# Optimization experiments

Hardware: AMD Instinct MI355X
Metric: run time of the kernel (lower is better)

The kernel has to match this reference:

```python
import jax, jax.numpy as jnp
import numpy as np

NEG_SLOPE = 0.2  # PyG GATConv default leaky_relu slope


def _gat_layer(x, W, att_src, att_dst, bias, src, dst, num_nodes, heads, out_c, concat):
    # x: [N, F_in] -> h: [N, H, C]
    h = (x @ W).reshape(num_nodes, heads, out_c)
    a_src = jnp.einsum('nhc,hc->nh', h, att_src)  # [N, H]
    a_dst = jnp.einsum('nhc,hc->nh', h, att_dst)  # [N, H]
    # edge (src -> dst): attention logit per edge/head
    e = jax.nn.leaky_relu(a_src[src] + a_dst[dst], NEG_SLOPE)  # [E, H]
    # softmax over edges sharing the same destination node
    m = jax.ops.segment_max(e, dst, num_segments=num_nodes)  # [N, H]
    m = jnp.where(jnp.isfinite(m), m, 0.0)
    ex = jnp.exp(e - m[dst])
    denom = jax.ops.segment_sum(ex, dst, num_segments=num_nodes)  # [N, H]
    alpha = ex / (denom[dst] + 1e-16)  # [E, H]
    # weighted scatter-add aggregation
    msg = h[src] * alpha[:, :, None]  # [E, H, C]
    out = jax.ops.segment_sum(msg, dst, num_segments=num_nodes)  # [N, H, C]
    if concat:
        out = out.reshape(num_nodes, heads * out_c)
    else:
        out = out.mean(axis=1)
    return out + bias


def _add_self_loops(edge_index, num_nodes):
    loop = jnp.arange(num_nodes, dtype=edge_index.dtype)
    src = jnp.concatenate([edge_index[0], loop])
    dst = jnp.concatenate([edge_index[1], loop])
    return src, dst


def setup_inputs() -> dict:
    key = jax.random.key(0)
    ks = jax.random.split(key, 9)
    N, F_in, E, H, C, OUT = 30000, 256, 300000, 8, 128, 64
    x = jax.random.normal(ks[0], (N, F_in), dtype=jnp.float32)
    edge_index = jax.random.randint(ks[1], (2, E), 0, N, dtype=jnp.int32)
    s1 = 1.0 / np.sqrt(F_in)
    s2 = 1.0 / np.sqrt(H * C)
    return {
        'x': x,
        'edge_index': edge_index,
        'W1': jax.random.normal(ks[2], (F_in, H * C), dtype=jnp.float32) * s1,
        'att_src1': jax.random.normal(ks[3], (H, C), dtype=jnp.float32) * s2,
        'att_dst1': jax.random.normal(ks[4], (H, C), dtype=jnp.float32) * s2,
        'b1': jnp.zeros((H * C,), dtype=jnp.float32),
        'W2': jax.random.normal(ks[5], (H * C, OUT), dtype=jnp.float32) * s2,
        'att_src2': jax.random.normal(ks[6], (1, OUT), dtype=jnp.float32) * 0.125,
        'att_dst2': jax.random.normal(ks[7], (1, OUT), dtype=jnp.float32) * 0.125,
        'b2': jnp.zeros((OUT,), dtype=jnp.float32),
    }


def reference(x, edge_index, W1, att_src1, att_dst1, b1, W2, att_src2, att_dst2, b2):
    N = x.shape[0]
    src, dst = _add_self_loops(edge_index, N)
    # dropout layers are identity in eval mode
    h = _gat_layer(x, W1, att_src1, att_dst1, b1, src, dst, N, 8, 128, True)
    h = jax.nn.elu(h)
    out = _gat_layer(h, W2, att_src2, att_dst2, b2, src, dst, N, 1, 64, False)
    return jax.nn.log_softmax(out, axis=-1)
```

## Files before the change

### kernel.cpp

```cpp
#include <hip/hip_runtime.h>
#include <math.h>

#define N_NODES 30000
#define F_IN 256
#define E_RAW 300000
#define E_TOT (E_RAW + N_NODES)
#define HEADS 8
#define CH 128
#define HC 1024
#define OUTC 64
#define NEG_SLOPE 0.2f
#define CAP 64

typedef __attribute__((ext_vector_type(8))) short bf16x8;
typedef __attribute__((ext_vector_type(4))) float f32x4;
typedef __attribute__((ext_vector_type(2))) float f32x2;

__device__ __forceinline__ float bf2f(unsigned short u) {
    return __uint_as_float(((unsigned)u) << 16);
}
__device__ __forceinline__ unsigned short f2bf(float f) {
    unsigned b = __float_as_uint(f);
    b += 0x7FFFu + ((b >> 16) & 1u);
    return (unsigned short)(b >> 16);
}
__device__ __forceinline__ void edge_sd(const int* __restrict__ ei, int e, int& s, int& d) {
    if (e < E_RAW) { s = ei[e]; d = ei[E_RAW + e]; }
    else           { s = e - E_RAW; d = s; }
}
__device__ __forceinline__ void async_cp16(const void* g, void* l) {
    __builtin_amdgcn_global_load_lds((const __attribute__((address_space(1))) void*)g,
                                     (__attribute__((address_space(3))) void*)l, 16, 0, 0);
}
__device__ __forceinline__ int slotP(int s) {
    return ((s >> 6) << 6) + ((s >> 2) & 15) + ((s & 3) << 4);
}
__device__ __forceinline__ void wave_sync() {
    __builtin_amdgcn_fence(__ATOMIC_ACQ_REL, "wavefront");
    __builtin_amdgcn_wave_barrier();
}

#define NB_CVTX (N_NODES * F_IN / 4 / 256)
#define NB_DEG  ((E_TOT + 255) / 256)
#define NB_W1T  ((F_IN * HC + 255) / 256)
#define NB_W2T  ((HC * OUTC + 255) / 256)
#define NB_PREP (NB_CVTX + NB_DEG + NB_W1T + NB_W2T)

__global__ __launch_bounds__(256)
void prep_kernel(const float* __restrict__ x, unsigned short* __restrict__ xb,
                 const float* __restrict__ W1, unsigned short* __restrict__ W1t,
                 const float* __restrict__ W2, unsigned short* __restrict__ W2t,
                 const int* __restrict__ ei, int* __restrict__ deg)
{
    const int b = blockIdx.x, t = threadIdx.x;
    if (b < NB_CVTX) {
        int i = b * 256 + t;
        const float4 v = reinterpret_cast<const float4*>(x)[i];
        ushort4 o;
        o.x = f2bf(v.x); o.y = f2bf(v.y); o.z = f2bf(v.z); o.w = f2bf(v.w);
        reinterpret_cast<ushort4*>(xb)[i] = o;
    } else if (b < NB_CVTX + NB_DEG) {
        int e = (b - NB_CVTX) * 256 + t;
        if (e < E_TOT) {
            int s, d; edge_sd(ei, e, s, d);
            atomicAdd(&deg[d], 1);
        }
    } else if (b < NB_CVTX + NB_DEG + NB_W1T) {
        int i = (b - NB_CVTX - NB_DEG) * 256 + t;
        if (i < F_IN * HC) {
            int k = i >> 10, n = i & (HC - 1);
            W1t[n * F_IN + k] = f2bf(W1[i]);
        }
    } else {
        int i = (b - NB_CVTX - NB_DEG - NB_W1T) * 256 + t;
        if (i < HC * OUTC) {
            int s = i >> 6, n = i & (OUTC - 1);
            W2t[n * HC + s] = f2bf(W2[slotP(s) * OUTC + n]);
        }
    }
}

__global__ __launch_bounds__(256)
void gemm1_mfma(const unsigned short* __restrict__ A,
                const unsigned short* __restrict__ Bt,
                unsigned* __restrict__ Cp,
                const float* __restrict__ att_src, const float* __restrict__ att_dst,
                float* __restrict__ a_src, float* __restrict__ a_dst, int M)
{
    __shared__ unsigned short Al[128 * 64];
    __shared__ unsigned short Bl[128 * 64];
    __shared__ float s_src[128][2];
    __shared__ float s_dst[128][2];
    const int tid  = threadIdx.x;
    const int wave = tid >> 6, lane = tid & 63;
    const int quad = lane >> 4, l16 = lane & 15;
    const int wr = (wave >> 1) * 64, wc = (wave & 1) * 64;
    const int row0 = blockIdx.y * 128;
    const int col0 = blockIdx.x * 128;

    f32x4 acc[4][4];
#pragma unroll
    for (int i = 0; i < 4; i++)
#pragma unroll
        for (int j = 0; j < 4; j++) acc[i][j] = (f32x4){0.f, 0.f, 0.f, 0.f};

    for (int k0 = 0; k0 < F_IN; k0 += 64) {
#pragma unroll
        for (int p = 0; p < 4; p++) {
            int idx = tid + 256 * p;
            int r = idx >> 3, q = idx & 7;
            async_cp16(A + (size_t)(row0 + r) * F_IN + k0 + ((q ^ (r & 7)) * 8),
                       Al + (size_t)(wave * 64 + 256 * p) * 8);
        }
#pragma unroll
        for (int p = 0; p < 4; p++) {
            int idx = tid + 256 * p;
            int r = idx >> 3, q = idx & 7;
            async_cp16(Bt + (size_t)(col0 + r) * F_IN + k0 + ((q ^ (r & 7)) * 8),
                       Bl + (size_t)(wave * 64 + 256 * p) * 8);
        }
        __syncthreads();
#pragma unroll
        for (int kh = 0; kh < 2; kh++) {
            const int cx = (kh * 4 + quad) ^ (l16 & 7);
            bf16x8 af[4], bg[4];
#pragma unroll
            for (int i = 0; i < 4; i++)
                af[i] = *reinterpret_cast<const bf16x8*>(Al + ((wr + i * 16 + l16) * 8 + cx) * 8);
#pragma unroll
            for (int j = 0; j < 4; j++)
                bg[j] = *reinterpret_cast<const bf16x8*>(Bl + ((wc + j * 16 + l16) * 8 + cx) * 8);
#pragma unroll
            for (int i = 0; i < 4; i++)
#pragma unroll
                for (int j = 0; j < 4; j++)
                    acc[i][j] = __builtin_amdgcn_mfma_f32_16x16x32_bf16(af[i], bg[j], acc[i][j], 0, 0, 0);
        }
        __syncthreads();
    }
    const int D = ((col0 + wc) >> 6) * 16 + l16;
#pragma unroll
    for (int i = 0; i < 4; i++) {
#pragma unroll
        for (int r = 0; r < 4; r++) {
            int row = row0 + wr + i * 16 + quad * 4 + r;
            if (row >= M) continue;
            int w8 = __builtin_amdgcn_cvt_pk_fp8_f32(acc[i][0][r], acc[i][1][r], 0, false);
            w8 = __builtin_amdgcn_cvt_pk_fp8_f32(acc[i][2][r], acc[i][3][r], w8, true);
            Cp[(size_t)row * 256 + D] = (unsigned)w8;
        }
    }
    const float* asv = att_src + blockIdx.x * CH;
    const float* adv = att_dst + blockIdx.x * CH;
    float av[4], dv[4];
#pragma unroll
    for (int j = 0; j < 4; j++) {
        av[j] = asv[wc + j * 16 + l16];
        dv[j] = adv[wc + j * 16 + l16];
    }
#pragma unroll
    for (int i = 0; i < 4; i++) {
#pragma unroll
        for (int r = 0; r < 4; r++) {
            float ps = 0.f, pd = 0.f;
#pragma unroll
            for (int j = 0; j < 4; j++) {
                float cc = acc[i][j][r];
                ps += cc * av[j];
                pd += cc * dv[j];
            }
#pragma unroll
            for (int o = 1; o < 16; o <<= 1) {
                ps += __shfl_xor(ps, o);
                pd += __shfl_xor(pd, o);
            }
            if (l16 == 0) {
                int lr = wr + i * 16 + quad * 4 + r;
                s_src[lr][wc >> 6] = ps;
                s_dst[lr][wc >> 6] = pd;
            }
        }
    }
    __syncthreads();
    if (tid < 128) {
        int row = row0 + tid;
        if (row < M) {
            a_src[row * 8 + blockIdx.x] = s_src[tid][0] + s_src[tid][1];
            a_dst[row * 8 + blockIdx.x] = s_dst[tid][0] + s_dst[tid][1];
        }
    }
}

__global__ __launch_bounds__(256)
void gemm2_mfma(const unsigned short* __restrict__ A,
                const unsigned short* __restrict__ Bt,
                unsigned short* __restrict__ C,
                const float* __restrict__ att_src2, const float* __restrict__ att_dst2,
                float* __restrict__ a_src2, float* __restrict__ a_dst2, int M)
{
    __shared__ unsigned short Al[64 * 64];
    __shared__ unsigned short Bl[64 * 64];
    const int tid  = threadIdx.x;
    const int wave = tid >> 6, lane = tid & 63;
    const int quad = lane >> 4, l16 = lane & 15;
    const int wr = wave * 16;
    const int row0 = blockIdx.x * 64;

    f32x4 acc[4];
#pragma unroll
    for (int j = 0; j < 4; j++) acc[j] = (f32x4){0.f, 0.f, 0.f, 0.f};

    for (int k0 = 0; k0 < HC; k0 += 64) {
#pragma unroll
        for (int p = 0; p < 2; p++) {
            int idx = tid + 256 * p;
            int r = idx >> 3, q = idx & 7;
            async_cp16(A + (size_t)(row0 + r) * HC + k0 + ((q ^ (r & 7)) * 8),
                       Al + (size_t)(wave * 64 + 256 * p) * 8);
        }
#pragma unroll
        for (int p = 0; p < 2; p++) {
            int idx = tid + 256 * p;
            int r = idx >> 3, q = idx & 7;
            async_cp16(Bt + (size_t)r * HC + k0 + ((q ^ (r & 7)) * 8),
                       Bl + (size_t)(wave * 64 + 256 * p) * 8);
        }
        __syncthreads();
#pragma unroll
        for (int kh = 0; kh < 2; kh++) {
            const int cx = (kh * 4 + quad) ^ (l16 & 7);
            bf16x8 af, bg[4];
            af = *reinterpret_cast<const bf16x8*>(Al + ((wr + l16) * 8 + cx) * 8);
#pragma unroll
            for (int j = 0; j < 4; j++)
                bg[j] = *reinterpret_cast<const bf16x8*>(Bl + ((j * 16 + l16) * 8 + cx) * 8);
#pragma unroll
            for (int j = 0; j < 4; j++)
                acc[j] = __builtin_amdgcn_mfma_f32_16x16x32_bf16(af, bg[j], acc[j], 0, 0, 0);
        }
        __syncthreads();
    }
    float av[4], dv[4];
#pragma unroll
    for (int j = 0; j < 4; j++) {
        av[j] = att_src2[j * 16 + l16];
        dv[j] = att_dst2[j * 16 + l16];
    }
#pragma unroll
    for (int r = 0; r < 4; r++) {
        int row = row0 + wr + quad * 4 + r;
        float ps = 0.f, pd = 0.f;
#pragma unroll
        for (int j = 0; j < 4; j++) {
            float cc = acc[j][r];
            int col = j * 16 + l16;
            if (row < M) C[(size_t)row * OUTC + col] = f2bf(cc);
            ps += cc * av[j];
            pd += cc * dv[j];
        }
#pragma unroll
        for (int o = 1; o < 16; o <<= 1) {
            ps += __shfl_xor(ps, o);
            pd += __shfl_xor(pd, o);
        }
        if (l16 == 0 && row < M) {
            a_src2[row] = ps;
            a_dst2[row] = pd;
        }
    }
}

__global__ __launch_bounds__(256)
void alloc_kernel(const int* __restrict__ deg, int* __restrict__ rowstart,
                  int* __restrict__ cursor, int* __restrict__ counter)
{
    int d = blockIdx.x * 256 + threadIdx.x;
    int lane = threadIdx.x & 63;
    int v = (d < N_NODES) ? deg[d] : 0;
    int x = v;
#pragma unroll
    for (int o = 1; o < 64; o <<= 1) {
        int y = __shfl_up(x, o);
        if (lane >= o) x += y;
    }
    int excl = x - v;
    int total = __shfl(x, 63);
    int base = 0;
    if (lane == 63) base = atomicAdd(counter, total);
    base = __shfl(base, 63);
    if (d < N_NODES) {
        rowstart[d] = base + excl;
        cursor[d]   = base + excl;
    }
}

__global__ void scatter_kernel(const int* __restrict__ ei, int* __restrict__ cursor,
                               int* __restrict__ csr_src)
{
    int e = blockIdx.x * 256 + threadIdx.x;
    if (e >= E_TOT) return;
    int s, d; edge_sd(ei, e, s, d);
    int pos = atomicAdd(&cursor[d], 1);
    csr_src[pos] = s;
}

__global__ __launch_bounds__(256)
void agg1_fused(const int* __restrict__ rowstart, const int* __restrict__ degv,
                const int* __restrict__ csr_src,
                const unsigned* __restrict__ h1p,
                const float* __restrict__ a_src1, const float* __restrict__ a_dst1,
                const float* __restrict__ b1, unsigned short* __restrict__ out1)
{
    const int t   = threadIdx.x;
    const int sub = t >> 6;
    const int tl  = t & 63;
    const int h   = tl >> 3;
    const int d   = blockIdx.x * 4 + sub;

    __shared__ float exps[4][CAP * 8];
    __shared__ int   srcs[4][CAP];

    const int start = rowstart[d];
    const int deg   = degv[d];

    const float adst = a_dst1[d * 8 + h];
    const uint4* __restrict__ h1v = reinterpret_cast<const uint4*>(h1p);

    float denom_part = 0.f;
    float acc[16];
#pragma unroll
    for (int k = 0; k < 16; k++) acc[k] = 0.f;

    for (int c0 = 0; c0 < deg; c0 += CAP) {
        const int cend = min(deg - c0, CAP);
        for (int c = (tl & 7); c < cend; c += 8) {
            int s = csr_src[start + c0 + c];
            if (h == 0) srcs[sub][c] = s;
            float a = a_src1[s * 8 + h] + adst;
            float v = a > 0.f ? a : NEG_SLOPE * a;
            float ex = __expf(v);
            exps[sub][c * 8 + h] = ex;
            denom_part += ex;
        }
        wave_sync();
        {
            int   s_cur = srcs[sub][0];
            float w_cur = exps[sub][h];
            uint4 u_cur = h1v[(size_t)s_cur * 64 + tl];
            for (int c = 0; c < cend; c++) {
                int   s_nxt = 0; float w_nxt = 0.f; uint4 u_nxt;
                if (c + 1 < cend) {
                    s_nxt = srcs[sub][c + 1];
                    w_nxt = exps[sub][(c + 1) * 8 + h];
                    u_nxt = h1v[(size_t)s_nxt * 64 + tl];
                }
#pragma unroll
                for (int dw = 0; dw < 4; dw++) {
                    unsigned wd = (&u_cur.x)[dw];
                    f32x2 lo = __builtin_amdgcn_cvt_pk_f32_fp8((int)wd, false);
                    f32x2 hi = __builtin_amdgcn_cvt_pk_f32_fp8((int)wd, true);
                    acc[dw * 4 + 0] += w_cur * lo.x;
                    acc[dw * 4 + 1] += w_cur * lo.y;
                    acc[dw * 4 + 2] += w_cur * hi.x;
                    acc[dw * 4 + 3] += w_cur * hi.y;
                }
                s_cur = s_nxt; w_cur = w_nxt; u_cur = u_nxt;
            }
        }
        wave_sync();
    }
#pragma unroll
    for (int o = 1; o < 8; o <<= 1) denom_part += __shfl_xor(denom_part, o);
    const float dinv = 1.f / (denom_part + 1e-16f);

    unsigned short ov[16];
#pragma unroll
    for (int e = 0; e < 16; e++) {
        float v = acc[e] * dinv + b1[slotP(16 * tl + e)];
        v = v > 0.f ? v : __expf(v) - 1.f;
        ov[e] = f2bf(v);
    }
    uint4* op = reinterpret_cast<uint4*>(out1 + (size_t)d * HC + 16 * tl);
    op[0] = *reinterpret_cast<uint4*>(&ov[0]);
    op[1] = *reinterpret_cast<uint4*>(&ov[8]);
}

__global__ __launch_bounds__(256)
void agg2_lsm(const int* __restrict__ rowstart, const int* __restrict__ degv,
              const int* __restrict__ csr_src,
              const unsigned short* __restrict__ h2,
              const float* __restrict__ a_src2, const float* __restrict__ a_dst2,
              const float* __restrict__ b2, float* __restrict__ out)
{
    const int t = threadIdx.x;
    const int sub  = t >> 6;
    const int lane = t & 63;
    const int eo   = lane >> 4;
    const int cq   = lane & 15;
    const int d = blockIdx.x * 4 + sub;

    __shared__ float exs[4][CAP];
    __shared__ int   ss[4][CAP];

    const int start = rowstart[d];
    const int deg   = degv[d];

    const float adst = a_dst2[d];
    const uint2* __restrict__ h2v = reinterpret_cast<const uint2*>(h2);
    float denom_part = 0.f;
    float ax = 0.f, ay = 0.f, az = 0.f, aw = 0.f;

    for (int c0 = 0; c0 < deg; c0 += CAP) {
        const int cend = min(deg - c0, CAP);
        for (int c = lane; c < cend; c += 64) {
            int s = csr_src[start + c0 + c];
            ss[sub][c] = s;
            float a = a_src2[s] + adst;
            float v = a > 0.f ? a : NEG_SLOPE * a;
            float ex = __expf(v);
            exs[sub][c] = ex;
            denom_part += ex;
        }
        wave_sync();
        {
            int   cc = eo;
            float w0 = (cc < cend) ? exs[sub][cc] : 0.f;
            int   s0 = (cc < cend) ? ss[sub][cc] : ss[sub][0];
            uint2 u0 = h2v[(size_t)s0 * 16 + cq];
            for (int c = 0; c + 4 < cend; c += 4) {
                int cc1 = c + 4 + eo;
                float w1 = (cc1 < cend) ? exs[sub][cc1] : 0.f;
                int   s1 = (cc1 < cend) ? ss[sub][cc1] : ss[sub][0];
                uint2 u1 = h2v[(size_t)s1 * 16 + cq];
                ax += w0 * __uint_as_float(u0.x << 16);
                ay += w0 * __uint_as_float(u0.x & 0xFFFF0000u);
                az += w0 * __uint_as_float(u0.y << 16);
                aw += w0 * __uint_as_float(u0.y & 0xFFFF0000u);
                w0 = w1; s0 = s1; u0 = u1;
            }
            ax += w0 * __uint_as_float(u0.x << 16);
            ay += w0 * __uint_as_float(u0.x & 0xFFFF0000u);
            az += w0 * __uint_as_float(u0.y << 16);
            aw += w0 * __uint_as_float(u0.y & 0xFFFF0000u);
        }
        wave_sync();
    }
    ax += __shfl_xor(ax, 16); ax += __shfl_xor(ax, 32);
    ay += __shfl_xor(ay, 16); ay += __shfl_xor(ay, 32);
    az += __shfl_xor(az, 16); az += __shfl_xor(az, 32);
    aw += __shfl_xor(aw, 16); aw += __shfl_xor(aw, 32);
#pragma unroll
    for (int o = 32; o > 0; o >>= 1) denom_part += __shfl_xor(denom_part, o);
    const float dinv = 1.f / (denom_part + 1e-16f);

    float4 bb = reinterpret_cast<const float4*>(b2)[cq];
    float v0 = ax * dinv + bb.x;
    float v1 = ay * dinv + bb.y;
    float v2 = az * dinv + bb.z;
    float v3 = aw * dinv + bb.w;
    float m = fmaxf(fmaxf(v0, v1), fmaxf(v2, v3));
#pragma unroll
    for (int o = 1; o < 16; o <<= 1) m = fmaxf(m, __shfl_xor(m, o));
    float ex = __expf(v0 - m) + __expf(v1 - m) + __expf(v2 - m) + __expf(v3 - m);
    float ssum = ex;
#pragma unroll
    for (int o = 1; o < 16; o <<= 1) ssum += __shfl_xor(ssum, o);
    if (eo == 0) {
        float lg = __logf(ssum);
        reinterpret_cast<float4*>(out + (size_t)d * OUTC)[cq] =
            make_float4(v0 - m - lg, v1 - m - lg, v2 - m - lg, v3 - m - lg);
    }
}

extern "C" void kernel_launch(void* const* d_in, const int* in_sizes, int n_in,
                              void* d_out, int out_size, void* d_ws, size_t ws_size,
                              hipStream_t stream)
{
    const float* x   = (const float*)d_in[0];
    const int*   ei  = (const int*)d_in[1];
    const float* W1  = (const float*)d_in[2];
    const float* as1 = (const float*)d_in[3];
    const float* ad1 = (const float*)d_in[4];
    const float* b1  = (const float*)d_in[5];
    const float* W2  = (const float*)d_in[6];
    const float* as2 = (const float*)d_in[7];
    const float* ad2 = (const float*)d_in[8];
    const float* b2  = (const float*)d_in[9];

    char* p = (char*)d_ws;
    auto alloc = [&](size_t bytes) { char* r = p; p += (bytes + 255) & ~(size_t)255; return r; };

    char* region0 = (char*)alloc((size_t)N_NODES * HC * 2);
    unsigned* h1p = (unsigned*)region0;

    char* region1 = (char*)alloc((size_t)N_NODES * HC * 2);
    unsigned short* out1 = (unsigned short*)region1;
    unsigned short* xb   = (unsigned short*)region1;
    unsigned short* W1t  = (unsigned short*)(region1 + (size_t)N_NODES * F_IN * 2 + 256);

    unsigned short* W2t = (unsigned short*)alloc((size_t)OUTC * HC * 2);

    float* a_src1   = (float*)alloc((size_t)N_NODES * HEADS * 4);
    float* a_dst1   = (float*)alloc((size_t)N_NODES * HEADS * 4);
    int*   deg      = (int*)alloc((size_t)(N_NODES + 1) * 4);
    int*   counter  = deg + N_NODES;
    int*   rowstart = (int*)alloc((size_t)N_NODES * 4);
    int*   cursor   = (int*)alloc((size_t)N_NODES * 4);
    int*   csr_src  = (int*)alloc((size_t)E_TOT * 4);

    char* q = region0;
    auto alias = [&](size_t bytes) { char* r = q; q += (bytes + 255) & ~(size_t)255; return r; };
    unsigned short* h2 = (unsigned short*)alias((size_t)N_NODES * OUTC * 2);
    float* a_src2  = (float*)alias((size_t)N_NODES * 4);
    float* a_dst2  = (float*)alias((size_t)N_NODES * 4);

    hipMemsetAsync(deg, 0, (size_t)(N_NODES + 1) * 4, stream);

    prep_kernel<<<NB_PREP, 256, 0, stream>>>(x, xb, W1, W1t, W2, W2t, ei, deg);

    alloc_kernel<<<(N_NODES + 255) / 256, 256, 0, stream>>>(deg, rowstart, cursor, counter);
    scatter_kernel<<<(E_TOT + 255) / 256, 256, 0, stream>>>(ei, cursor, csr_src);

    gemm1_mfma<<<dim3(HC / 128, (N_NODES + 127) / 128), 256, 0, stream>>>(
        xb, W1t, h1p, as1, ad1, a_src1, a_dst1, N_NODES);
    agg1_fused<<<N_NODES / 4, 256, 0, stream>>>(rowstart, deg, csr_src, h1p, a_src1, a_dst1, b1, out1);

    gemm2_mfma<<<(N_NODES + 63) / 64, 256, 0, stream>>>(
        out1, W2t, h2, as2, ad2, a_src2, a_dst2, N_NODES);
    agg2_lsm<<<N_NODES / 4, 256, 0, stream>>>(rowstart, deg, csr_src, h2, a_src2, a_dst2, b2, (float*)d_out);
}
```

Before: 259.0 us.

## Aggregate raw inputs per head before the layer-1 projection GEMM

Layer 1 is reordered algebraically. The attention logits now come straight from x through W1·att vectors precomputed in a small kernel. Each destination node aggregates fp8 copies of the 256-wide input per head into a 2048-wide buffer, and a per-head GEMM then applies W1, bias and ELU. This removes the large fp8 1024-wide hidden feature tensor and its gather traffic, in exchange for a bigger per-head aggregated buffer and a GEMM whose K spans per-head slices. Logits are scaled by log2e so exp2 can be used, and the softmax max-subtraction is dropped, which risks overflow for large logits.

```diff
diff --git a/kernel.cpp b/kernel.cpp
--- a/kernel.cpp
+++ b/kernel.cpp
@@ -11,14 +11,13 @@
 #define OUTC 64
 #define NEG_SLOPE 0.2f
 #define CAP 64
+#define LOG2E 1.44269504f
+#define MPAD 30080
 
 typedef __attribute__((ext_vector_type(8))) short bf16x8;
 typedef __attribute__((ext_vector_type(4))) float f32x4;
 typedef __attribute__((ext_vector_type(2))) float f32x2;
 
-__device__ __forceinline__ float bf2f(unsigned short u) {
-    return __uint_as_float(((unsigned)u) << 16);
-}
 __device__ __forceinline__ unsigned short f2bf(float f) {
     unsigned b = __float_as_uint(f);
     b += 0x7FFFu + ((b >> 16) & 1u);
@@ -32,33 +31,71 @@
     __builtin_amdgcn_global_load_lds((const __attribute__((address_space(1))) void*)g,
                                      (__attribute__((address_space(3))) void*)l, 16, 0, 0);
 }
-__device__ __forceinline__ int slotP(int s) {
-    return ((s >> 6) << 6) + ((s >> 2) & 15) + ((s & 3) << 4);
-}
 __device__ __forceinline__ void wave_sync() {
     __builtin_amdgcn_fence(__ATOMIC_ACQ_REL, "wavefront");
     __builtin_amdgcn_wave_barrier();
 }
 
-#define NB_CVTX (N_NODES * F_IN / 4 / 256)
+__global__ __launch_bounds__(256)
+void vsrc_kernel(const float* __restrict__ W1, const float* __restrict__ att_src,
+                 const float* __restrict__ att_dst, float* __restrict__ vsd)
+{
+    const int j = blockIdx.x;
+    const int k = threadIdx.x;
+    const int hj = j & 7;
+    const float* av = (j < 8 ? att_src : att_dst) + hj * CH;
+    const float* wr = W1 + (size_t)k * HC + hj * CH;
+    float s = 0.f;
+#pragma unroll 4
+    for (int c = 0; c < CH; c += 4)
+        s += wr[c] * av[c] + wr[c + 1] * av[c + 1] + wr[c + 2] * av[c + 2] + wr[c + 3] * av[c + 3];
+    vsd[j * 256 + k] = s;
+}
+
+#define NB_CVTX (N_NODES / 16)
 #define NB_DEG  ((E_TOT + 255) / 256)
 #define NB_W1T  ((F_IN * HC + 255) / 256)
 #define NB_W2T  ((HC * OUTC + 255) / 256)
 #define NB_PREP (NB_CVTX + NB_DEG + NB_W1T + NB_W2T)
 
 __global__ __launch_bounds__(256)
-void prep_kernel(const float* __restrict__ x, unsigned short* __restrict__ xb,
+void prep_kernel(const float* __restrict__ x, unsigned* __restrict__ x8,
                  const float* __restrict__ W1, unsigned short* __restrict__ W1t,
                  const float* __restrict__ W2, unsigned short* __restrict__ W2t,
-                 const int* __restrict__ ei, int* __restrict__ deg)
+                 const int* __restrict__ ei, int* __restrict__ deg,
+                 const float* __restrict__ vsd,
+                 float* __restrict__ a_src1, float* __restrict__ a_dst1)
 {
     const int b = blockIdx.x, t = threadIdx.x;
     if (b < NB_CVTX) {
-        int i = b * 256 + t;
-        const float4 v = reinterpret_cast<const float4*>(x)[i];
-        ushort4 o;
-        o.x = f2bf(v.x); o.y = f2bf(v.y); o.z = f2bf(v.z); o.w = f2bf(v.w);
-        reinterpret_cast<ushort4*>(xb)[i] = o;
+        const int w = t >> 6, l = t & 63;
+        const int n0 = b * 16 + w * 4;
+        float4 vs[16];
+        const float4* vs4 = reinterpret_cast<const float4*>(vsd);
+#pragma unroll
+        for (int j = 0; j < 16; j++) vs[j] = vs4[j * 64 + l];
+#pragma unroll 1
+        for (int nn = 0; nn < 4; nn++) {
+            const int n = n0 + nn;
+            const float4 v = reinterpret_cast<const float4*>(x)[(size_t)n * 64 + l];
+            unsigned xd = __builtin_amdgcn_cvt_pk_fp8_f32(v.x, v.y, 0, false);
+            xd = (unsigned)__builtin_amdgcn_cvt_pk_fp8_f32(v.z, v.w, (int)xd, true);
+            x8[(size_t)n * 64 + l] = xd;
+            float pp[16];
+#pragma unroll
+            for (int j = 0; j < 16; j++)
+                pp[j] = v.x * vs[j].x + v.y * vs[j].y + v.z * vs[j].z + v.w * vs[j].w;
+#pragma unroll
+            for (int o = 1; o < 64; o <<= 1)
+#pragma unroll
+                for (int j = 0; j < 16; j++) pp[j] += __shfl_xor(pp[j], o);
+            float sel = pp[0];
+#pragma unroll
+            for (int j = 1; j < 16; j++) if (l == j) sel = pp[j];
+            sel *= LOG2E;
+            if (l < 8)       a_src1[n * 8 + l] = sel;
+            else if (l < 16) a_dst1[n * 8 + (l - 8)] = sel;
+        }
     } else if (b < NB_CVTX + NB_DEG) {
         int e = (b - NB_CVTX) * 256 + t;
         if (e < E_TOT) {
@@ -74,198 +111,8 @@
     } else {
         int i = (b - NB_CVTX - NB_DEG - NB_W1T) * 256 + t;
         if (i < HC * OUTC) {
-            int s = i >> 6, n = i & (OUTC - 1);
-            W2t[n * HC + s] = f2bf(W2[slotP(s) * OUTC + n]);
-        }
-    }
-}
-
-__global__ __launch_bounds__(256)
-void gemm1_mfma(const unsigned short* __restrict__ A,
-                const unsigned short* __restrict__ Bt,
-                unsigned* __restrict__ Cp,
-                const float* __restrict__ att_src, const float* __restrict__ att_dst,
-                float* __restrict__ a_src, float* __restrict__ a_dst, int M)
-{
-    __shared__ unsigned short Al[128 * 64];
-    __shared__ unsigned short Bl[128 * 64];
-    __shared__ float s_src[128][2];
-    __shared__ float s_dst[128][2];
-    const int tid  = threadIdx.x;
-    const int wave = tid >> 6, lane = tid & 63;
-    const int quad = lane >> 4, l16 = lane & 15;
-    const int wr = (wave >> 1) * 64, wc = (wave & 1) * 64;
-    const int row0 = blockIdx.y * 128;
-    const int col0 = blockIdx.x * 128;
-
-    f32x4 acc[4][4];
-#pragma unroll
-    for (int i = 0; i < 4; i++)
-#pragma unroll
-        for (int j = 0; j < 4; j++) acc[i][j] = (f32x4){0.f, 0.f, 0.f, 0.f};
-
-    for (int k0 = 0; k0 < F_IN; k0 += 64) {
-#pragma unroll
-        for (int p = 0; p < 4; p++) {
-            int idx = tid + 256 * p;
-            int r = idx >> 3, q = idx & 7;
-            async_cp16(A + (size_t)(row0 + r) * F_IN + k0 + ((q ^ (r & 7)) * 8),
-                       Al + (size_t)(wave * 64 + 256 * p) * 8);
-        }
-#pragma unroll
-        for (int p = 0; p < 4; p++) {
-            int idx = tid + 256 * p;
-            int r = idx >> 3, q = idx & 7;
-            async_cp16(Bt + (size_t)(col0 + r) * F_IN + k0 + ((q ^ (r & 7)) * 8),
-                       Bl + (size_t)(wave * 64 + 256 * p) * 8);
-        }
-        __syncthreads();
-#pragma unroll
-        for (int kh = 0; kh < 2; kh++) {
-            const int cx = (kh * 4 + quad) ^ (l16 & 7);
-            bf16x8 af[4], bg[4];
-#pragma unroll
-            for (int i = 0; i < 4; i++)
-                af[i] = *reinterpret_cast<const bf16x8*>(Al + ((wr + i * 16 + l16) * 8 + cx) * 8);
-#pragma unroll
-            for (int j = 0; j < 4; j++)
-                bg[j] = *reinterpret_cast<const bf16x8*>(Bl + ((wc + j * 16 + l16) * 8 + cx) * 8);
-#pragma unroll
-            for (int i = 0; i < 4; i++)
-#pragma unroll
-                for (int j = 0; j < 4; j++)
-                    acc[i][j] = __builtin_amdgcn_mfma_f32_16x16x32_bf16(af[i], bg[j], acc[i][j], 0, 0, 0);
-        }
-        __syncthreads();
-    }
-    const int D = ((col0 + wc) >> 6) * 16 + l16;
-#pragma unroll
-    for (int i = 0; i < 4; i++) {
-#pragma unroll
-        for (int r = 0; r < 4; r++) {
-            int row = row0 + wr + i * 16 + quad * 4 + r;
-            if (row >= M) continue;
-            int w8 = __builtin_amdgcn_cvt_pk_fp8_f32(acc[i][0][r], acc[i][1][r], 0, false);
-            w8 = __builtin_amdgcn_cvt_pk_fp8_f32(acc[i][2][r], acc[i][3][r], w8, true);
-            Cp[(size_t)row * 256 + D] = (unsigned)w8;
-        }
-    }
-    const float* asv = att_src + blockIdx.x * CH;
-    const float* adv = att_dst + blockIdx.x * CH;
-    float av[4], dv[4];
-#pragma unroll
-    for (int j = 0; j < 4; j++) {
-        av[j] = asv[wc + j * 16 + l16];
-        dv[j] = adv[wc + j * 16 + l16];
-    }
-#pragma unroll
-    for (int i = 0; i < 4; i++) {
-#pragma unroll
-        for (int r = 0; r < 4; r++) {
-            float ps = 0.f, pd = 0.f;
-#pragma unroll
-            for (int j = 0; j < 4; j++) {
-                float cc = acc[i][j][r];
-                ps += cc * av[j];
-                pd += cc * dv[j];
-            }
-#pragma unroll
-            for (int o = 1; o < 16; o <<= 1) {
-                ps += __shfl_xor(ps, o);
-                pd += __shfl_xor(pd, o);
-            }
-            if (l16 == 0) {
-                int lr = wr + i * 16 + quad * 4 + r;
-                s_src[lr][wc >> 6] = ps;
-                s_dst[lr][wc >> 6] = pd;
-            }
-        }
-    }
-    __syncthreads();
-    if (tid < 128) {
-        int row = row0 + tid;
-        if (row < M) {
-            a_src[row * 8 + blockIdx.x] = s_src[tid][0] + s_src[tid][1];
-            a_dst[row * 8 + blockIdx.x] = s_dst[tid][0] + s_dst[tid][1];
-        }
-    }
-}
-
-__global__ __launch_bounds__(256)
-void gemm2_mfma(const unsigned short* __restrict__ A,
-                const unsigned short* __restrict__ Bt,
-                unsigned short* __restrict__ C,
-                const float* __restrict__ att_src2, const float* __restrict__ att_dst2,
-                float* __restrict__ a_src2, float* __restrict__ a_dst2, int M)
-{
-    __shared__ unsigned short Al[64 * 64];
-    __shared__ unsigned short Bl[64 * 64];
-    const int tid  = threadIdx.x;
-    const int wave = tid >> 6, lane = tid & 63;
-    const int quad = lane >> 4, l16 = lane & 15;
-    const int wr = wave * 16;
-    const int row0 = blockIdx.x * 64;
-
-    f32x4 acc[4];
-#pragma unroll
-    for (int j = 0; j < 4; j++) acc[j] = (f32x4){0.f, 0.f, 0.f, 0.f};
-
-    for (int k0 = 0; k0 < HC; k0 += 64) {
-#pragma unroll
-        for (int p = 0; p < 2; p++) {
-            int idx = tid + 256 * p;
-            int r = idx >> 3, q = idx & 7;
-            async_cp16(A + (size_t)(row0 + r) * HC + k0 + ((q ^ (r & 7)) * 8),
-                       Al + (size_t)(wave * 64 + 256 * p) * 8);
-        }
-#pragma unroll
-        for (int p = 0; p < 2; p++) {
-            int idx = tid + 256 * p;
-            int r = idx >> 3, q = idx & 7;
-            async_cp16(Bt + (size_t)r * HC + k0 + ((q ^ (r & 7)) * 8),
-                       Bl + (size_t)(wave * 64 + 256 * p) * 8);
-        }
-        __syncthreads();
-#pragma unroll
-        for (int kh = 0; kh < 2; kh++) {
-            const int cx = (kh * 4 + quad) ^ (l16 & 7);
-            bf16x8 af, bg[4];
-            af = *reinterpret_cast<const bf16x8*>(Al + ((wr + l16) * 8 + cx) * 8);
-#pragma unroll
-            for (int j = 0; j < 4; j++)
-                bg[j] = *reinterpret_cast<const bf16x8*>(Bl + ((j * 16 + l16) * 8 + cx) * 8);
-#pragma unroll
-            for (int j = 0; j < 4; j++)
-                acc[j] = __builtin_amdgcn_mfma_f32_16x16x32_bf16(af, bg[j], acc[j], 0, 0, 0);
-        }
-        __syncthreads();
-    }
-    float av[4], dv[4];
-#pragma unroll
-    for (int j = 0; j < 4; j++) {
-        av[j] = att_src2[j * 16 + l16];
-        dv[j] = att_dst2[j * 16 + l16];
-    }
-#pragma unroll
-    for (int r = 0; r < 4; r++) {
-        int row = row0 + wr + quad * 4 + r;
-        float ps = 0.f, pd = 0.f;
-#pragma unroll
-        for (int j = 0; j < 4; j++) {
-            float cc = acc[j][r];
-            int col = j * 16 + l16;
-            if (row < M) C[(size_t)row * OUTC + col] = f2bf(cc);
-            ps += cc * av[j];
-            pd += cc * dv[j];
-        }
-#pragma unroll
-        for (int o = 1; o < 16; o <<= 1) {
-            ps += __shfl_xor(ps, o);
-            pd += __shfl_xor(pd, o);
-        }
-        if (l16 == 0 && row < M) {
-            a_src2[row] = ps;
-            a_dst2[row] = pd;
+            int k = i >> 6, n = i & (OUTC - 1);
+            W2t[n * HC + k] = f2bf(W2[k * OUTC + n]);
         }
     }
 }
@@ -304,85 +151,260 @@
     csr_src[pos] = s;
 }
 
-__global__ __launch_bounds__(256)
-void agg1_fused(const int* __restrict__ rowstart, const int* __restrict__ degv,
-                const int* __restrict__ csr_src,
-                const unsigned* __restrict__ h1p,
-                const float* __restrict__ a_src1, const float* __restrict__ a_dst1,
-                const float* __restrict__ b1, unsigned short* __restrict__ out1)
+struct GX4 { int s[4]; };
+struct VX4 { float a[4]; unsigned x[4]; };
+
+__device__ __forceinline__ GX4 gx4_load(const int* __restrict__ csr, int start, int c, int dm) {
+    GX4 g;
+#pragma unroll
+    for (int j = 0; j < 4; j++) g.s[j] = csr[start + min(c + j, dm)];
+    return g;
+}
+__device__ __forceinline__ VX4 vx4_load(const float* __restrict__ a_src1,
+                                        const unsigned* __restrict__ x8,
+                                        GX4 g, int hh, int tl) {
+    VX4 r;
+#pragma unroll
+    for (int j = 0; j < 4; j++) {
+        r.a[j] = a_src1[g.s[j] * 8 + hh];
+        r.x[j] = x8[(size_t)g.s[j] * 64 + tl];
+    }
+    return r;
+}
+
+#define XEDGE(lg_, xd_) do { \
+    float v_ = fmaxf((lg_), NEG_SLOPE * (lg_)); \
+    float w_ = __builtin_amdgcn_exp2f(v_); \
+    dn += w_; \
+    float wh_[8]; \
+    _Pragma("unroll") \
+    for (int q_ = 0; q_ < 8; q_++) wh_[q_] = __shfl(w_, lb | q_); \
+    f32x2 lo_ = __builtin_amdgcn_cvt_pk_f32_fp8((int)(xd_), false); \
+    f32x2 hi_ = __builtin_amdgcn_cvt_pk_f32_fp8((int)(xd_), true); \
+    _Pragma("unroll") \
+    for (int q_ = 0; q_ < 8; q_++) { \
+        acc[q_][0] += wh_[q_] * lo_.x; \
+        acc[q_][1] += wh_[q_] * lo_.y; \
+        acc[q_][2] += wh_[q_] * hi_.x; \
+        acc[q_][3] += wh_[q_] * hi_.y; \
+    } \
+} while (0)
+
+__global__ __launch_bounds__(256)
+void aggx_kernel(const int* __restrict__ rowstart, const int* __restrict__ degv,
+                 const int* __restrict__ csr_src,
+                 const unsigned* __restrict__ x8,
+                 const float* __restrict__ a_src1, const float* __restrict__ a_dst1,
+                 unsigned short* __restrict__ aggx)
 {
     const int t   = threadIdx.x;
     const int sub = t >> 6;
     const int tl  = t & 63;
-    const int h   = tl >> 3;
+    const int hh  = tl & 7;
+    const int lb  = tl & 56;
     const int d   = blockIdx.x * 4 + sub;
 
-    __shared__ float exps[4][CAP * 8];
-    __shared__ int   srcs[4][CAP];
-
-    const int start = rowstart[d];
-    const int deg   = degv[d];
-
-    const float adst = a_dst1[d * 8 + h];
-    const uint4* __restrict__ h1v = reinterpret_cast<const uint4*>(h1p);
-
-    float denom_part = 0.f;
-    float acc[16];
-#pragma unroll
-    for (int k = 0; k < 16; k++) acc[k] = 0.f;
-
-    for (int c0 = 0; c0 < deg; c0 += CAP) {
-        const int cend = min(deg - c0, CAP);
-        for (int c = (tl & 7); c < cend; c += 8) {
-            int s = csr_src[start + c0 + c];
-            if (h == 0) srcs[sub][c] = s;
-            float a = a_src1[s * 8 + h] + adst;
-            float v = a > 0.f ? a : NEG_SLOPE * a;
-            float ex = __expf(v);
-            exps[sub][c * 8 + h] = ex;
-            denom_part += ex;
-        }
-        wave_sync();
-        {
-            int   s_cur = srcs[sub][0];
-            float w_cur = exps[sub][h];
-            uint4 u_cur = h1v[(size_t)s_cur * 64 + tl];
-            for (int c = 0; c < cend; c++) {
-                int   s_nxt = 0; float w_nxt = 0.f; uint4 u_nxt;
-                if (c + 1 < cend) {
-                    s_nxt = srcs[sub][c + 1];
-                    w_nxt = exps[sub][(c + 1) * 8 + h];
-                    u_nxt = h1v[(size_t)s_nxt * 64 + tl];
-                }
-#pragma unroll
-                for (int dw = 0; dw < 4; dw++) {
-                    unsigned wd = (&u_cur.x)[dw];
-                    f32x2 lo = __builtin_amdgcn_cvt_pk_f32_fp8((int)wd, false);
-                    f32x2 hi = __builtin_amdgcn_cvt_pk_f32_fp8((int)wd, true);
-                    acc[dw * 4 + 0] += w_cur * lo.x;
-                    acc[dw * 4 + 1] += w_cur * lo.y;
-                    acc[dw * 4 + 2] += w_cur * hi.x;
-                    acc[dw * 4 + 3] += w_cur * hi.y;
-                }
-                s_cur = s_nxt; w_cur = w_nxt; u_cur = u_nxt;
+    const int start = __builtin_amdgcn_readfirstlane(rowstart[d]);
+    const int deg   = __builtin_amdgcn_readfirstlane(degv[d]);
+    const int dm    = deg - 1;
+    const float adst = a_dst1[d * 8 + hh];
+
+    float dn = 0.f;
+    float acc[8][4];
+#pragma unroll
+    for (int h = 0; h < 8; h++)
+#pragma unroll
+        for (int k = 0; k < 4; k++) acc[h][k] = 0.f;
+
+    GX4 sC = gx4_load(csr_src, start, 0, dm);
+    VX4 vC = vx4_load(a_src1, x8, sC, hh, tl);
+    GX4 sN = gx4_load(csr_src, start, 4, dm);
+
+#pragma unroll 1
+    for (int c = 0; c < deg; c += 4) {
+        const bool more = (c + 4 < deg);
+        VX4 vN;
+        if (more) { vN = vx4_load(a_src1, x8, sN, hh, tl); sN = gx4_load(csr_src, start, c + 8, dm); }
+        if (c + 4 <= deg) {
+            XEDGE(vC.a[0] + adst, vC.x[0]);
+            XEDGE(vC.a[1] + adst, vC.x[1]);
+            XEDGE(vC.a[2] + adst, vC.x[2]);
+            XEDGE(vC.a[3] + adst, vC.x[3]);
+        } else {
+            float l0 = (c + 0 < deg) ? vC.a[0] + adst : -1e30f; XEDGE(l0, vC.x[0]);
+            float l1 = (c + 1 < deg) ? vC.a[1] + adst : -1e30f; XEDGE(l1, vC.x[1]);
+            float l2 = (c + 2 < deg) ? vC.a[2] + adst : -1e30f; XEDGE(l2, vC.x[2]);
+            float l3 = (c + 3 < deg) ? vC.a[3] + adst : -1e30f; XEDGE(l3, vC.x[3]);
+        }
+        if (more) vC = vN;
+    }
+
+    const float dinv = 1.f / (dn + 1e-16f);
+    unsigned short* ag = aggx + (size_t)d * 2048 + 4 * tl;
+#pragma unroll
+    for (int h = 0; h < 8; h++) {
+        float di = __shfl(dinv, lb | h);
+        ushort4 o;
+        o.x = f2bf(acc[h][0] * di);
+        o.y = f2bf(acc[h][1] * di);
+        o.z = f2bf(acc[h][2] * di);
+        o.w = f2bf(acc[h][3] * di);
+        *reinterpret_cast<ushort4*>(ag + h * 256) = o;
+    }
+}
+
+__global__ __launch_bounds__(256)
+void gemm1b(const unsigned short* __restrict__ A,
+            const unsigned short* __restrict__ Bt,
+            const float* __restrict__ b1,
+            unsigned short* __restrict__ out1, int M)
+{
+    __shared__ unsigned short Al[128 * 64];
+    __shared__ unsigned short Bl[128 * 64];
+    const int tid  = threadIdx.x;
+    const int wave = tid >> 6, lane = tid & 63;
+    const int quad = lane >> 4, l16 = lane & 15;
+    const int wr = (wave >> 1) * 64, wc = (wave & 1) * 64;
+    const int row0 = blockIdx.y * 128;
+    const int col0 = blockIdx.x * 128;
+    const int ak0  = blockIdx.x * 256;
+
+    f32x4 acc[4][4];
+#pragma unroll
+    for (int i = 0; i < 4; i++)
+#pragma unroll
+        for (int j = 0; j < 4; j++) acc[i][j] = (f32x4){0.f, 0.f, 0.f, 0.f};
+
+    for (int k0 = 0; k0 < F_IN; k0 += 64) {
+#pragma unroll
+        for (int p = 0; p < 4; p++) {
+            int idx = tid + 256 * p;
+            int r = idx >> 3, q = idx & 7;
+            async_cp16(A + (size_t)(row0 + r) * 2048 + ak0 + k0 + ((q ^ (r & 7)) * 8),
+                       Al + (size_t)(wave * 64 + 256 * p) * 8);
+        }
+#pragma unroll
+        for (int p = 0; p < 4; p++) {
+            int idx = tid + 256 * p;
+            int r = idx >> 3, q = idx & 7;
+            async_cp16(Bt + (size_t)(col0 + r) * F_IN + k0 + ((q ^ (r & 7)) * 8),
+                       Bl + (size_t)(wave * 64 + 256 * p) * 8);
+        }
+        __syncthreads();
+#pragma unroll
+        for (int kh = 0; kh < 2; kh++) {
+            const int cx = (kh * 4 + quad) ^ (l16 & 7);
+            bf16x8 af[4], bg[4];
+#pragma unroll
+            for (int i = 0; i < 4; i++)
+                af[i] = *reinterpret_cast<const bf16x8*>(Al + ((wr + i * 16 + l16) * 8 + cx) * 8);
+#pragma unroll
+            for (int j = 0; j < 4; j++)
+                bg[j] = *reinterpret_cast<const bf16x8*>(Bl + ((wc + j * 16 + l16) * 8 + cx) * 8);
+#pragma unroll
+            for (int i = 0; i < 4; i++)
+#pragma unroll
+                for (int j = 0; j < 4; j++)
+                    acc[i][j] = __builtin_amdgcn_mfma_f32_16x16x32_bf16(af[i], bg[j], acc[i][j], 0, 0, 0);
+        }
+        __syncthreads();
+    }
+    float bb[4];
+#pragma unroll
+    for (int j = 0; j < 4; j++) bb[j] = b1[col0 + wc + j * 16 + l16];
+#pragma unroll
+    for (int i = 0; i < 4; i++) {
+#pragma unroll
+        for (int r = 0; r < 4; r++) {
+            int row = row0 + wr + i * 16 + quad * 4 + r;
+            if (row >= M) continue;
+#pragma unroll
+            for (int j = 0; j < 4; j++) {
+                float v = acc[i][j][r] + bb[j];
+                v = v > 0.f ? v : __expf(v) - 1.f;
+                out1[(size_t)row * HC + col0 + wc + j * 16 + l16] = f2bf(v);
             }
         }
-        wave_sync();
-    }
-#pragma unroll
-    for (int o = 1; o < 8; o <<= 1) denom_part += __shfl_xor(denom_part, o);
-    const float dinv = 1.f / (denom_part + 1e-16f);
-
-    unsigned short ov[16];
-#pragma unroll
-    for (int e = 0; e < 16; e++) {
-        float v = acc[e] * dinv + b1[slotP(16 * tl + e)];
-        v = v > 0.f ? v : __expf(v) - 1.f;
-        ov[e] = f2bf(v);
-    }
-    uint4* op = reinterpret_cast<uint4*>(out1 + (size_t)d * HC + 16 * tl);
-    op[0] = *reinterpret_cast<uint4*>(&ov[0]);
-    op[1] = *reinterpret_cast<uint4*>(&ov[8]);
+    }
+}
+
+__global__ __launch_bounds__(256)
+void gemm2_mfma(const unsigned short* __restrict__ A,
+                const unsigned short* __restrict__ Bt,
+                unsigned short* __restrict__ C,
+                const float* __restrict__ att_src2, const float* __restrict__ att_dst2,
+                float* __restrict__ a_src2, float* __restrict__ a_dst2, int M)
+{
+    __shared__ unsigned short Al[64 * 64];
+    __shared__ unsigned short Bl[64 * 64];
+    const int tid  = threadIdx.x;
+    const int wave = tid >> 6, lane = tid & 63;
+    const int quad = lane >> 4, l16 = lane & 15;
+    const int wr = wave * 16;
+    const int row0 = blockIdx.x * 64;
+
+    f32x4 acc[4];
+#pragma unroll
+    for (int j = 0; j < 4; j++) acc[j] = (f32x4){0.f, 0.f, 0.f, 0.f};
+
+    for (int k0 = 0; k0 < HC; k0 += 64) {
+#pragma unroll
+        for (int p = 0; p < 2; p++) {
+            int idx = tid + 256 * p;
+            int r = idx >> 3, q = idx & 7;
+            async_cp16(A + (size_t)(row0 + r) * HC + k0 + ((q ^ (r & 7)) * 8),
+                       Al + (size_t)(wave * 64 + 256 * p) * 8);
+        }
+#pragma unroll
+        for (int p = 0; p < 2; p++) {
+            int idx = tid + 256 * p;
+            int r = idx >> 3, q = idx & 7;
+            async_cp16(Bt + (size_t)r * HC + k0 + ((q ^ (r & 7)) * 8),
+                       Bl + (size_t)(wave * 64 + 256 * p) * 8);
+        }
+        __syncthreads();
+#pragma unroll
+        for (int kh = 0; kh < 2; kh++) {
+            const int cx = (kh * 4 + quad) ^ (l16 & 7);
+            bf16x8 af, bg[4];
+            af = *reinterpret_cast<const bf16x8*>(Al + ((wr + l16) * 8 + cx) * 8);
+#pragma unroll
+            for (int j = 0; j < 4; j++)
+                bg[j] = *reinterpret_cast<const bf16x8*>(Bl + ((j * 16 + l16) * 8 + cx) * 8);
+#pragma unroll
+            for (int j = 0; j < 4; j++)
+                acc[j] = __builtin_amdgcn_mfma_f32_16x16x32_bf16(af, bg[j], acc[j], 0, 0, 0);
+        }
+        __syncthreads();
+    }
+    float av[4], dv[4];
+#pragma unroll
+    for (int j = 0; j < 4; j++) {
+        av[j] = att_src2[j * 16 + l16];
+        dv[j] = att_dst2[j * 16 + l16];
+    }
+#pragma unroll
+    for (int r = 0; r < 4; r++) {
+        int row = row0 + wr + quad * 4 + r;
+        float ps = 0.f, pd = 0.f;
+#pragma unroll
+        for (int j = 0; j < 4; j++) {
+            float cc = acc[j][r];
+            int col = j * 16 + l16;
+            if (row < M) C[(size_t)row * OUTC + col] = f2bf(cc);
+            ps += cc * av[j];
+            pd += cc * dv[j];
+        }
+#pragma unroll
+        for (int o = 1; o < 16; o <<= 1) {
+            ps += __shfl_xor(ps, o);
+            pd += __shfl_xor(pd, o);
+        }
+        if (l16 == 0 && row < M) {
+            a_src2[row] = ps;
+            a_dst2[row] = pd;
+        }
+    }
 }
 
 __global__ __launch_bounds__(256)
@@ -490,15 +512,16 @@
     char* p = (char*)d_ws;
     auto alloc = [&](size_t bytes) { char* r = p; p += (bytes + 255) & ~(size_t)255; return r; };
 
-    char* region0 = (char*)alloc((size_t)N_NODES * HC * 2);
-    unsigned* h1p = (unsigned*)region0;
-
-    char* region1 = (char*)alloc((size_t)N_NODES * HC * 2);
-    unsigned short* out1 = (unsigned short*)region1;
-    unsigned short* xb   = (unsigned short*)region1;
-    unsigned short* W1t  = (unsigned short*)(region1 + (size_t)N_NODES * F_IN * 2 + 256);
-
+    char* regionP = (char*)alloc((size_t)MPAD * 2048 * 2);
+    unsigned short* aggx = (unsigned short*)regionP;
+
+    char* regionQ = (char*)alloc((size_t)(N_NODES + 16) * HC * 2);
+    unsigned short* out1 = (unsigned short*)regionQ;
+    unsigned* x8 = (unsigned*)regionQ;
+
+    unsigned short* W1t = (unsigned short*)alloc((size_t)F_IN * HC * 2);
     unsigned short* W2t = (unsigned short*)alloc((size_t)OUTC * HC * 2);
+    float* vsd = (float*)alloc(16 * 256 * 4);
 
     float* a_src1   = (float*)alloc((size_t)N_NODES * HEADS * 4);
     float* a_dst1   = (float*)alloc((size_t)N_NODES * HEADS * 4);
@@ -508,7 +531,7 @@
     int*   cursor   = (int*)alloc((size_t)N_NODES * 4);
     int*   csr_src  = (int*)alloc((size_t)E_TOT * 4);
 
-    char* q = region0;
+    char* q = regionP;
     auto alias = [&](size_t bytes) { char* r = q; q += (bytes + 255) & ~(size_t)255; return r; };
     unsigned short* h2 = (unsigned short*)alias((size_t)N_NODES * OUTC * 2);
     float* a_src2  = (float*)alias((size_t)N_NODES * 4);
@@ -516,14 +539,17 @@
 
     hipMemsetAsync(deg, 0, (size_t)(N_NODES + 1) * 4, stream);
 
-    prep_kernel<<<NB_PREP, 256, 0, stream>>>(x, xb, W1, W1t, W2, W2t, ei, deg);
+    vsrc_kernel<<<16, 256, 0, stream>>>(W1, as1, ad1, vsd);
+
+    prep_kernel<<<NB_PREP, 256, 0, stream>>>(x, x8, W1, W1t, W2, W2t, ei, deg,
+                                             vsd, a_src1, a_dst1);
 
     alloc_kernel<<<(N_NODES + 255) / 256, 256, 0, stream>>>(deg, rowstart, cursor, counter);
     scatter_kernel<<<(E_TOT + 255) / 256, 256, 0, stream>>>(ei, cursor, csr_src);
 
-    gemm1_mfma<<<dim3(HC / 128, (N_NODES + 127) / 128), 256, 0, stream>>>(
-        xb, W1t, h1p, as1, ad1, a_src1, a_dst1, N_NODES);
-    agg1_fused<<<N_NODES / 4, 256, 0, stream>>>(rowstart, deg, csr_src, h1p, a_src1, a_dst1, b1, out1);
+    aggx_kernel<<<N_NODES / 4, 256, 0, stream>>>(rowstart, deg, csr_src, x8,
+                                                 a_src1, a_dst1, aggx);
+    gemm1b<<<dim3(HEADS, (N_NODES + 127) / 128), 256, 0, stream>>>(aggx, W1t, b1, out1, N_NODES);
 
     gemm2_mfma<<<(N_NODES + 63) / 64, 256, 0, stream>>>(
         out1, W2t, h2, as2, ad2, a_src2, a_dst2, N_NODES);
```

New measurement: 288.2 us. 11.3% more time.
